# Optimization experiments

Measured on AMD Instinct MI355X. Metric: run time of the kernel, lower is better.

Reference implementation:

```python
import jax, jax.numpy as jnp
import numpy as np

D_MODEL = 256
N_HEADS = 8
D_FF = 1024
N_LAYERS = 6
INPUT_DIM = 2
EPS = 1e-5  # torch LayerNorm default


def _layer_norm(x, g, b):
    m = jnp.mean(x, axis=-1, keepdims=True)
    v = jnp.mean((x - m) ** 2, axis=-1, keepdims=True)
    return (x - m) / jnp.sqrt(v + EPS) * g + b


def setup_inputs() -> dict:
    key = jax.random.key(0)
    ks = jax.random.split(key, 8)
    f32 = jnp.float32

    def w(k, shape, fan_in):
        return jax.random.normal(k, shape, f32) * (1.0 / np.sqrt(fan_in))

    return {
        "x": jax.random.normal(ks[0], (8, 1024, INPUT_DIM), f32),
        "in_w": w(ks[1], (INPUT_DIM, D_MODEL), INPUT_DIM),
        "in_b": jnp.zeros((D_MODEL,), f32),
        "ln1_g": jnp.ones((D_MODEL,), f32),
        "ln1_b": jnp.zeros((D_MODEL,), f32),
        "qkv_w": w(ks[2], (D_MODEL, 3 * D_MODEL), D_MODEL),
        "qkv_b": jnp.zeros((3 * D_MODEL,), f32),
        "out_w": w(ks[3], (D_MODEL, D_MODEL), D_MODEL),
        "out_b": jnp.zeros((D_MODEL,), f32),
        "lna_g": jnp.ones((D_MODEL,), f32),
        "lna_b": jnp.zeros((D_MODEL,), f32),
        "ln2_g": jnp.ones((D_MODEL,), f32),
        "ln2_b": jnp.zeros((D_MODEL,), f32),
        "ff1_w": w(ks[4], (D_MODEL, D_FF), D_MODEL),
        "ff1_b": jnp.zeros((D_FF,), f32),
        "ff2_w": w(ks[5], (D_FF, D_MODEL), D_FF),
        "ff2_b": jnp.zeros((D_MODEL,), f32),
        "lnf_g": jnp.ones((D_MODEL,), f32),
        "lnf_b": jnp.zeros((D_MODEL,), f32),
    }


def reference(x, in_w, in_b, ln1_g, ln1_b, qkv_w, qkv_b, out_w, out_b,
              lna_g, lna_b, ln2_g, ln2_b, ff1_w, ff1_b, ff2_w, ff2_b,
              lnf_g, lnf_b):
    B, L, _ = x.shape
    dk = D_MODEL // N_HEADS
    scale = 1.0 / np.sqrt(dk)
    top_k = max(1, L // 4)

    # sinusoidal positional encoding [L, D]
    pos = jnp.arange(L, dtype=jnp.float32)[:, None]
    div = jnp.exp(jnp.arange(0, D_MODEL, 2, dtype=jnp.float32)
                  * (-np.log(10000.0) / D_MODEL))
    pe = jnp.zeros((L, D_MODEL), jnp.float32)
    pe = pe.at[:, 0::2].set(jnp.sin(pos * div))
    pe = pe.at[:, 1::2].set(jnp.cos(pos * div))

    h = x @ in_w + in_b + pe[None]  # [B, L, D]

    # VoformerEncoder reuses the SAME layer object -> shared weights, 6 passes
    for _ in range(N_LAYERS):
        # --- self-attention sublayer (pre-norm) ---
        s2 = _layer_norm(h, ln1_g, ln1_b)
        qkv = (s2 @ qkv_w + qkv_b).reshape(B, L, 3, N_HEADS, dk)
        q = qkv[:, :, 0].transpose(0, 2, 1, 3)  # [B, H, L, dk]
        k = qkv[:, :, 1].transpose(0, 2, 1, 3)
        v = qkv[:, :, 2].transpose(0, 2, 1, 3)

        scores = jnp.einsum('bhqd,bhkd->bhqk', q, k) * scale  # [B,H,L,L]
        # ProbSparse: keep only the per-row top-k scores
        thr = jax.lax.top_k(scores, top_k)[0][..., -1:]
        sparse = jnp.where(scores >= thr, scores, -jnp.inf)
        attn = jax.nn.softmax(sparse, axis=-1)
        o = jnp.einsum('bhqk,bhkd->bhqd', attn, v)
        o = o.transpose(0, 2, 1, 3).reshape(B, L, D_MODEL)
        o = o @ out_w + out_b
        # InformerAttention applies its own residual + LayerNorm
        attn_out = _layer_norm(o + s2, lna_g, lna_b)
        h = h + attn_out

        # --- FFN sublayer with Volatilite activation ---
        s2 = _layer_norm(h, ln2_g, ln2_b)
        f = s2 @ ff1_w + ff1_b  # [B, L, d_ff]
        mean_f = jnp.mean(f, axis=1, keepdims=True)
        vol = jnp.sqrt(jnp.mean((mean_f - f) ** 2, axis=1, keepdims=True))
        f = f * vol
        f = f @ ff2_w + ff2_b
        h = h + f

    return _layer_norm(h, lnf_g, lnf_b)
```

## Files before the change

kernel.cpp:

```cpp
#include <hip/hip_runtime.h>
#include <math.h>

#define D_MODEL 256
#define NH 8
#define DFF 1024
#define NLAYERS 6
#define B_ 8
#define L_ 1024
#define NR (B_*L_)
#define TOPK 256
#define LNEPS 1e-5f

typedef __attribute__((ext_vector_type(8))) short bf16x8;
typedef __attribute__((ext_vector_type(4))) float f32x4;

__device__ __forceinline__ float wsum(float v){
  #pragma unroll
  for(int o=32;o>0;o>>=1) v += __shfl_xor(v,o,64);
  return v;
}
__device__ __forceinline__ float wmax(float v){
  #pragma unroll
  for(int o=32;o>0;o>>=1) v = fmaxf(v,__shfl_xor(v,o,64));
  return v;
}
__device__ __forceinline__ short f2bf(float x){
  unsigned u = __float_as_uint(x);
  u += 0x7fffu + ((u>>16)&1u);
  return (short)(u>>16);
}
__device__ __forceinline__ float bf2f(short s){
  return __uint_as_float(((unsigned)(unsigned short)s)<<16);
}
__device__ __forceinline__ void g2l(const short* g, short* l){
  __builtin_amdgcn_global_load_lds(
      (const __attribute__((address_space(1))) unsigned int*)g,
      (__attribute__((address_space(3))) unsigned int*)l,
      16, 0, 0);
}

__global__ __launch_bounds__(256) void embed_kernel(
    const float* __restrict__ x, const float* __restrict__ in_w,
    const float* __restrict__ in_b, float* __restrict__ h)
{
  int tid = blockIdx.x*256 + threadIdx.x;
  int n  = tid >> 6;
  int d0 = (tid & 63) << 2;
  int l  = n & (L_-1);
  float x0 = x[2*n], x1 = x[2*n+1];
  const float kf = -0.07195578415606394f;
  float pe[4];
  #pragma unroll
  for(int ii=0; ii<2; ++ii){
    int i = (d0>>1) + ii;
    float dv  = expf((float)i * kf);
    float ang = (float)l * dv;
    pe[2*ii]   = sinf(ang);
    pe[2*ii+1] = cosf(ang);
  }
  float4 w0 = *(const float4*)(in_w + d0);
  float4 w1 = *(const float4*)(in_w + D_MODEL + d0);
  float4 bb = *(const float4*)(in_b + d0);
  float4 o;
  o.x = x0*w0.x + x1*w1.x + bb.x + pe[0];
  o.y = x0*w0.y + x1*w1.y + bb.y + pe[1];
  o.z = x0*w0.z + x1*w1.z + bb.z + pe[2];
  o.w = x0*w0.w + x1*w1.w + bb.w + pe[3];
  *(float4*)(h + (size_t)n*D_MODEL + d0) = o;
}

__global__ __launch_bounds__(256) void wcvt(
    const float* __restrict__ W, short* __restrict__ WT, int N, int kshift)
{
  int idx = blockIdx.x*256 + threadIdx.x;
  int K = 1<<kshift;
  if (idx >= N*K) return;
  int n = idx >> kshift, k = idx & (K-1);
  WT[idx] = f2bf(W[(size_t)k*N + n]);
}

template<int OM>
__global__ __launch_bounds__(256) void ln_kernel(
    const float* __restrict__ in, const float* __restrict__ g,
    const float* __restrict__ b, float* __restrict__ out,
    short* __restrict__ outb)
{
  int wave = threadIdx.x >> 6, lane = threadIdx.x & 63;
  int row = blockIdx.x*4 + wave;
  float4 v = ((const float4*)(in + (size_t)row*D_MODEL))[lane];
  float s  = v.x+v.y+v.z+v.w;
  float sq = v.x*v.x+v.y*v.y+v.z*v.z+v.w*v.w;
  s = wsum(s); sq = wsum(sq);
  float mean = s*(1.f/D_MODEL);
  float var  = sq*(1.f/D_MODEL) - mean*mean;
  float rstd = 1.f/sqrtf(var + LNEPS);
  float4 gv = ((const float4*)g)[lane];
  float4 bv = ((const float4*)b)[lane];
  float4 o;
  o.x = (v.x-mean)*rstd*gv.x + bv.x;
  o.y = (v.y-mean)*rstd*gv.y + bv.y;
  o.z = (v.z-mean)*rstd*gv.z + bv.z;
  o.w = (v.w-mean)*rstd*gv.w + bv.w;
  if (OM == 0 || OM == 1){
    ((float4*)(out + (size_t)row*D_MODEL))[lane] = o;
  }
  if (OM == 3){
    float4* op = (float4*)(out + (size_t)row*D_MODEL) + lane;
    float4 hv = *op;
    o.x+=hv.x; o.y+=hv.y; o.z+=hv.z; o.w+=hv.w;
    *op = o;
  }
  if (OM == 1 || OM == 2){
    short4 s4; s4.x=f2bf(o.x); s4.y=f2bf(o.y); s4.z=f2bf(o.z); s4.w=f2bf(o.w);
    *(short4*)(outb + (size_t)row*D_MODEL + lane*4) = s4;
  }
}

template<int MODE>
__global__ __launch_bounds__(256) void mfma_gemm(
    const short* __restrict__ A, const short* __restrict__ BT,
    const float* __restrict__ bias, const float* __restrict__ resid,
    float* __restrict__ Cf, short* __restrict__ Cb, short* __restrict__ Vt,
    int N, int K)
{
  __shared__ __align__(16) short As[128*32];
  __shared__ __align__(16) short Bs[64*32];
  const int t = threadIdx.x, wv = t>>6, lane = t&63;
  const int r16 = lane&15, quad = lane>>4;
  const int m0 = blockIdx.y*128, n0 = blockIdx.x*64;
  const int ia0 = wv*128 + lane, ia1 = ia0 + 64;
  const int ib  = wv*64 + lane;
  const short* Ab = A  + (size_t)m0*K;
  const short* Bb = BT + (size_t)n0*K;
  const f32x4 z = {0.f,0.f,0.f,0.f};
  f32x4 acc[2][4];
  #pragma unroll
  for (int i=0;i<2;++i)
    #pragma unroll
    for (int j=0;j<4;++j) acc[i][j] = z;

  for (int k0 = 0; k0 < K; k0 += 32){
    __syncthreads();
    g2l(Ab + (size_t)(ia0>>2)*K + k0 + (ia0&3)*8, As + ia0*8);
    g2l(Ab + (size_t)(ia1>>2)*K + k0 + (ia1&3)*8, As + ia1*8);
    g2l(Bb + (size_t)(ib>>2)*K  + k0 + (ib&3)*8,  Bs + ib*8);
    __syncthreads();
    bf16x8 af0 = *(const bf16x8*)(As + ((wv*32      + r16)*32 + quad*8));
    bf16x8 af1 = *(const bf16x8*)(As + ((wv*32 + 16 + r16)*32 + quad*8));
    bf16x8 bf[4];
    #pragma unroll
    for (int ct=0; ct<4; ++ct)
      bf[ct] = *(const bf16x8*)(Bs + ((ct*16 + r16)*32 + quad*8));
    #pragma unroll
    for (int ct=0; ct<4; ++ct){
      acc[0][ct] = __builtin_amdgcn_mfma_f32_16x16x32_bf16(af0, bf[ct], acc[0][ct], 0,0,0);
      acc[1][ct] = __builtin_amdgcn_mfma_f32_16x16x32_bf16(af1, bf[ct], acc[1][ct], 0,0,0);
    }
  }

  #pragma unroll
  for (int rt=0; rt<2; ++rt){
    const int mb = m0 + wv*32 + rt*16 + quad*4;
    #pragma unroll
    for (int ct=0; ct<4; ++ct){
      const int n = n0 + ct*16 + r16;
      const float bv = bias[n];
      if (MODE == 0){
        if (n < 512){
          int region = n>>8, hh = (n>>5)&7, d = n&31;
          #pragma unroll
          for (int r=0;r<4;++r){
            int l = mb + r;
            size_t base = (((size_t)(region*64 + (l>>10)*8 + hh))*1024 + (l&1023))*32 + d;
            Cb[base] = f2bf(acc[rt][ct][r] + bv);
          }
        } else {
          int dv = n - 512, hh = dv>>5, d = dv&31;
          int b = mb>>10, lloc = mb&1023;
          size_t base = (((size_t)(b*8 + hh))*32 + d)*1024 + lloc;
          short4 s4;
          s4.x = f2bf(acc[rt][ct][0] + bv); s4.y = f2bf(acc[rt][ct][1] + bv);
          s4.z = f2bf(acc[rt][ct][2] + bv); s4.w = f2bf(acc[rt][ct][3] + bv);
          *(short4*)(Vt + base) = s4;
        }
      } else {
        #pragma unroll
        for (int r=0;r<4;++r){
          size_t off = (size_t)(mb + r)*N + n;
          float c = acc[rt][ct][r] + bv;
          if (MODE == 1) Cf[off] = c + resid[off];
          if (MODE == 2) Cb[off] = f2bf(c);
          if (MODE == 3) Cf[off] += c;
        }
      }
    }
  }
}

__global__ __launch_bounds__(256,4) void attn_mfma(
    const short* __restrict__ qkbf, const short* __restrict__ vT,
    short* __restrict__ ob)
{
  __shared__ __align__(16) short sc16[16*1024];
  const int t = threadIdx.x, wv = t>>6, lane = t&63;
  const int r16 = lane&15, quad = lane>>4;
  const int bh = blockIdx.x >> 6, qt = blockIdx.x & 63;

  bf16x8 aq = *(const bf16x8*)(qkbf + ((size_t)bh*1024 + qt*16 + r16)*32 + quad*8);
  const short* kb = qkbf + (size_t)(64 + bh)*1024*32;

  bf16x8 bk[16];
  #pragma unroll
  for (int tt=0; tt<16; ++tt)
    bk[tt] = *(const bf16x8*)(kb + (size_t)(wv*256 + tt*16 + r16)*32 + quad*8);
  #pragma unroll
  for (int tt=0; tt<16; ++tt){
    f32x4 c = {0.f,0.f,0.f,0.f};
    c = __builtin_amdgcn_mfma_f32_16x16x32_bf16(aq, bk[tt], c, 0, 0, 0);
    int key = wv*256 + tt*16 + r16;
    #pragma unroll
    for (int r=0;r<4;++r){
      int row = quad*4 + r;
      sc16[row*1024 + (key ^ ((row&7)<<3))] = f2bf(c[r]);
    }
  }
  __syncthreads();

  const float SC2 = 0.25500529485087056f;
  for (int rr=0; rr<4; ++rr){
    int row = wv*4 + rr;
    int s = (row&7)<<3;
    float scv[16]; int key[16];
    #pragma unroll
    for (int i=0;i<16;++i){
      short hsh = sc16[row*1024 + ((i*64+lane) ^ s)];
      scv[i] = bf2f(hsh);
      int u = (int)(unsigned short)hsh;
      key[i] = (u & 0x8000) ? (u ^ 0xFFFF) : (u | 0x8000);
    }
    int lo=0, hi=65536;
    while (hi - lo > 1){
      int mid = (lo+hi)>>1;
      int cnt = 0;
      #pragma unroll
      for (int i=0;i<16;++i)
        cnt += (int)__popcll(__ballot(key[i] >= mid));
      if (cnt >= TOPK) lo = mid; else hi = mid;
    }
    const int thr = lo;
    float mx = scv[0];
    #pragma unroll
    for (int i=1;i<16;++i) mx = fmaxf(mx, scv[i]);
    mx = wmax(mx);
    float sum = 0.f, w[16];
    #pragma unroll
    for (int i=0;i<16;++i){
      float e = (key[i] >= thr) ? exp2f((scv[i]-mx)*SC2) : 0.f;
      w[i] = e; sum += e;
    }
    sum = wsum(sum);
    const float inv = 1.f/sum;
    #pragma unroll
    for (int i=0;i<16;++i)
      sc16[row*1024 + ((i*64+lane) ^ s)] = f2bf(w[i]*inv);
  }
  __syncthreads();

  const short* vb = vT + (size_t)bh*32*1024;
  bf16x8 bvv[16];
  #pragma unroll
  for (int tt=0; tt<8; ++tt){
    int k0 = wv*256 + tt*32;
    #pragma unroll
    for (int n=0;n<2;++n)
      bvv[tt*2+n] = *(const bf16x8*)(vb + (size_t)(n*16 + r16)*1024 + k0 + quad*8);
  }
  f32x4 oa0 = {0.f,0.f,0.f,0.f}, oa1 = {0.f,0.f,0.f,0.f};
  #pragma unroll
  for (int tt=0; tt<8; ++tt){
    int k0 = wv*256 + tt*32;
    bf16x8 af = *(const bf16x8*)(sc16 + r16*1024 + ((k0 + quad*8) ^ ((r16&7)<<3)));
    oa0 = __builtin_amdgcn_mfma_f32_16x16x32_bf16(af, bvv[tt*2+0], oa0, 0, 0, 0);
    oa1 = __builtin_amdgcn_mfma_f32_16x16x32_bf16(af, bvv[tt*2+1], oa1, 0, 0, 0);
  }
  __syncthreads();
  float* po = (float*)sc16;
  #pragma unroll
  for (int r=0;r<4;++r){
    po[wv*512 + (quad*4+r)*32 +      r16] = oa0[r];
    po[wv*512 + (quad*4+r)*32 + 16 + r16] = oa1[r];
  }
  __syncthreads();
  int e = t*2;
  float v0 = po[e]   + po[512+e]   + po[1024+e]   + po[1536+e];
  float v1 = po[e+1] + po[512+e+1] + po[1024+e+1] + po[1536+e+1];
  int q = e>>5, d = e&31;
  int b = bh>>3, hh = bh&7;
  size_t off = ((size_t)(b*1024 + qt*16 + q))*256 + hh*32 + d;
  short2 s2o; s2o.x = f2bf(v0); s2o.y = f2bf(v1);
  *(short2*)(ob + off) = s2o;
}

__global__ __launch_bounds__(512) void vol_scale(short* __restrict__ f)
{
  __shared__ float ps[8][64], pq[8][64], vs[64];
  int b = blockIdx.x >> 4, cb = blockIdx.x & 15;
  int cl = threadIdx.x & 63, sl = threadIdx.x >> 6;
  int col = cb*64 + cl;
  short* fb = f + (size_t)b*L_*DFF + col;
  float s = 0.f, sq = 0.f;
  for (int l = sl*128; l < sl*128+128; ++l){
    float v = bf2f(fb[(size_t)l*DFF]);
    s += v; sq += v*v;
  }
  ps[sl][cl] = s; pq[sl][cl] = sq;
  __syncthreads();
  if (threadIdx.x < 64){
    float st=0.f, qt=0.f;
    #pragma unroll
    for (int i=0;i<8;++i){ st += ps[i][cl]; qt += pq[i][cl]; }
    float mean = st*(1.f/L_);
    float var  = qt*(1.f/L_) - mean*mean;
    vs[cl] = sqrtf(fmaxf(var, 0.f));
  }
  __syncthreads();
  float vv = vs[cl];
  for (int l = sl*128; l < sl*128+128; ++l){
    size_t o = (size_t)l*DFF;
    fb[o] = f2bf(bf2f(fb[o]) * vv);
  }
}

extern "C" void kernel_launch(void* const* d_in, const int* in_sizes, int n_in,
                              void* d_out, int out_size, void* d_ws, size_t ws_size,
                              hipStream_t stream) {
  const float* x     = (const float*)d_in[0];
  const float* in_w  = (const float*)d_in[1];
  const float* in_b  = (const float*)d_in[2];
  const float* ln1_g = (const float*)d_in[3];
  const float* ln1_b = (const float*)d_in[4];
  const float* qkv_w = (const float*)d_in[5];
  const float* qkv_b = (const float*)d_in[6];
  const float* out_w = (const float*)d_in[7];
  const float* out_b = (const float*)d_in[8];
  const float* lna_g = (const float*)d_in[9];
  const float* lna_b = (const float*)d_in[10];
  const float* ln2_g = (const float*)d_in[11];
  const float* ln2_b = (const float*)d_in[12];
  const float* ff1_w = (const float*)d_in[13];
  const float* ff1_b = (const float*)d_in[14];
  const float* ff2_w = (const float*)d_in[15];
  const float* ff2_b = (const float*)d_in[16];
  const float* lnf_g = (const float*)d_in[17];
  const float* lnf_b = (const float*)d_in[18];
  float* out = (float*)d_out;

  char* ws = (char*)d_ws;
  float* h     = (float*)(ws);
  float* s2    = (float*)(ws + (size_t)( 8<<20));
  short* s2b   = (short*)(ws + (size_t)(16<<20));
  short* qkbf  = (short*)(ws + (size_t)(20<<20));
  short* vTb   = (short*)(ws + (size_t)(28<<20));
  short* ob_b  = (short*)(ws + (size_t)(32<<20));
  short* f     = (short*)(ws + (size_t)(20<<20));
  float* tb    = (float*)(ws + (size_t)(36<<20));
  short* qkvwT = (short*)(ws + (size_t)(45<<20));
  short* outwT = (short*)(ws + (size_t)(45<<20) + 393216);
  short* ff1wT = (short*)(ws + (size_t)(45<<20) + 393216 + 131072);
  short* ff2wT = (short*)(ws + (size_t)(45<<20) + 393216 + 131072 + 524288);

  embed_kernel<<<NR*64/256, 256, 0, stream>>>(x, in_w, in_b, h);
  wcvt<<< 768, 256, 0, stream>>>(qkv_w, qkvwT,  768, 8);
  wcvt<<< 256, 256, 0, stream>>>(out_w, outwT,  256, 8);
  wcvt<<<1024, 256, 0, stream>>>(ff1_w, ff1wT, 1024, 8);
  wcvt<<<1024, 256, 0, stream>>>(ff2_w, ff2wT,  256, 10);

  for (int layer = 0; layer < NLAYERS; ++layer){
    ln_kernel<1><<<NR/4, 256, 0, stream>>>(h, ln1_g, ln1_b, s2, s2b);
    {
      dim3 g(768/64, NR/128);
      mfma_gemm<0><<<g, 256, 0, stream>>>(s2b, qkvwT, qkv_b, nullptr,
                                          nullptr, qkbf, vTb, 768, 256);
    }
    attn_mfma<<<64*64, 256, 0, stream>>>(qkbf, vTb, ob_b);
    {
      dim3 g(256/64, NR/128);
      mfma_gemm<1><<<g, 256, 0, stream>>>(ob_b, outwT, out_b, s2,
                                          tb, nullptr, nullptr, 256, 256);
    }
    ln_kernel<3><<<NR/4, 256, 0, stream>>>(tb, lna_g, lna_b, h, nullptr);
    ln_kernel<2><<<NR/4, 256, 0, stream>>>(h, ln2_g, ln2_b, nullptr, s2b);
    {
      dim3 g(1024/64, NR/128);
      mfma_gemm<2><<<g, 256, 0, stream>>>(s2b, ff1wT, ff1_b, nullptr,
                                          nullptr, f, nullptr, 1024, 256);
    }
    vol_scale<<<B_*16, 512, 0, stream>>>(f);
    {
      dim3 g(256/64, NR/128);
      mfma_gemm<3><<<g, 256, 0, stream>>>(f, ff2wT, ff2_b, nullptr,
                                          h, nullptr, nullptr, 256, 1024);
    }
  }
  ln_kernel<0><<<NR/4, 256, 0, stream>>>(h, lnf_g, lnf_b, out, nullptr);
}
```

Measured before the change: 1.362 ms.

## Fuse out-projection with residual and both LayerNorms, restructure top-k softmax attention

A new gemm_ln kernel does the attention output projection, adds the residual, applies the attention LayerNorm, adds the result into h and computes the next LN2 in its epilogue. This replaces one GEMM plus two LayerNorm launches and drops the fp32 s2 buffer; the residual is now read from the bf16 normalized input. The attention kernel now has each wave process four rows at once. It uses a 16-step bitwise threshold search on integer sort keys with interleaved ballots, defers softmax normalization to the PV output, stores scores in a transposed swizzled layout and remaps block indices. Risks: precision loss from the bf16 residual, and gemm_ln launches only 128 blocks with a non-pipelined K loop.

```diff
diff --git a/kernel.cpp b/kernel.cpp
--- a/kernel.cpp
+++ b/kernel.cpp
@@ -1,4 +1,5 @@
 #include <hip/hip_runtime.h>
+#include <hip/hip_bf16.h>
 #include <math.h>
 
 #define D_MODEL 256
@@ -19,11 +20,6 @@
   for(int o=32;o>0;o>>=1) v += __shfl_xor(v,o,64);
   return v;
 }
-__device__ __forceinline__ float wmax(float v){
-  #pragma unroll
-  for(int o=32;o>0;o>>=1) v = fmaxf(v,__shfl_xor(v,o,64));
-  return v;
-}
 __device__ __forceinline__ short f2bf(float x){
   unsigned u = __float_as_uint(x);
   u += 0x7fffu + ((u>>16)&1u);
@@ -31,6 +27,18 @@
 }
 __device__ __forceinline__ float bf2f(short s){
   return __uint_as_float(((unsigned)(unsigned short)s)<<16);
+}
+__device__ __forceinline__ unsigned pk2bf(float a, float b){
+  __hip_bfloat162 h = __float22bfloat162_rn(make_float2(a,b));
+  unsigned u; __builtin_memcpy(&u, &h, 4);
+  return u;
+}
+__device__ __forceinline__ int sortkey(unsigned u){
+  return (u & 0x8000u) ? (int)(u ^ 0xFFFFu) : (int)(u | 0x8000u);
+}
+__device__ __forceinline__ float kinvf(int k){
+  unsigned u = (k & 0x8000) ? ((unsigned)k ^ 0x8000u) : ((unsigned)k ^ 0xFFFFu);
+  return __uint_as_float(u << 16);
 }
 __device__ __forceinline__ void g2l(const short* g, short* l){
   __builtin_amdgcn_global_load_lds(
@@ -101,25 +109,19 @@
   o.y = (v.y-mean)*rstd*gv.y + bv.y;
   o.z = (v.z-mean)*rstd*gv.z + bv.z;
   o.w = (v.w-mean)*rstd*gv.w + bv.w;
-  if (OM == 0 || OM == 1){
+  if (OM == 0){
     ((float4*)(out + (size_t)row*D_MODEL))[lane] = o;
   }
-  if (OM == 3){
-    float4* op = (float4*)(out + (size_t)row*D_MODEL) + lane;
-    float4 hv = *op;
-    o.x+=hv.x; o.y+=hv.y; o.z+=hv.z; o.w+=hv.w;
-    *op = o;
-  }
-  if (OM == 1 || OM == 2){
-    short4 s4; s4.x=f2bf(o.x); s4.y=f2bf(o.y); s4.z=f2bf(o.z); s4.w=f2bf(o.w);
-    *(short4*)(outb + (size_t)row*D_MODEL + lane*4) = s4;
+  if (OM == 2){
+    uint2 pk; pk.x = pk2bf(o.x, o.y); pk.y = pk2bf(o.z, o.w);
+    *(uint2*)(outb + (size_t)row*D_MODEL + lane*4) = pk;
   }
 }
 
 template<int MODE>
 __global__ __launch_bounds__(256) void mfma_gemm(
     const short* __restrict__ A, const short* __restrict__ BT,
-    const float* __restrict__ bias, const float* __restrict__ resid,
+    const float* __restrict__ bias,
     float* __restrict__ Cf, short* __restrict__ Cb, short* __restrict__ Vt,
     int N, int K)
 {
@@ -178,17 +180,16 @@
           int dv = n - 512, hh = dv>>5, d = dv&31;
           int b = mb>>10, lloc = mb&1023;
           size_t base = (((size_t)(b*8 + hh))*32 + d)*1024 + lloc;
-          short4 s4;
-          s4.x = f2bf(acc[rt][ct][0] + bv); s4.y = f2bf(acc[rt][ct][1] + bv);
-          s4.z = f2bf(acc[rt][ct][2] + bv); s4.w = f2bf(acc[rt][ct][3] + bv);
-          *(short4*)(Vt + base) = s4;
+          uint2 pk;
+          pk.x = pk2bf(acc[rt][ct][0] + bv, acc[rt][ct][1] + bv);
+          pk.y = pk2bf(acc[rt][ct][2] + bv, acc[rt][ct][3] + bv);
+          *(uint2*)(Vt + base) = pk;
         }
       } else {
         #pragma unroll
         for (int r=0;r<4;++r){
           size_t off = (size_t)(mb + r)*N + n;
           float c = acc[rt][ct][r] + bv;
-          if (MODE == 1) Cf[off] = c + resid[off];
           if (MODE == 2) Cb[off] = f2bf(c);
           if (MODE == 3) Cf[off] += c;
         }
@@ -197,6 +198,85 @@
   }
 }
 
+template<int RES>
+__global__ __launch_bounds__(256) void gemm_ln(
+    const short* __restrict__ A, const short* __restrict__ BT,
+    const float* __restrict__ bias, const short* __restrict__ residb,
+    const float* __restrict__ ga, const float* __restrict__ ba,
+    const float* __restrict__ g2, const float* __restrict__ b2,
+    float* __restrict__ h, short* __restrict__ s2b, int K)
+{
+  __shared__ __align__(16) short As[64*32];
+  __shared__ __align__(16) short Bs[256*32];
+  const int t = threadIdx.x, wv = t>>6, lane = t&63;
+  const int r16 = lane&15, quad = lane>>4;
+  const int m0 = blockIdx.x*64;
+  const short* Ab = A + (size_t)m0*K;
+  const f32x4 z = {0.f,0.f,0.f,0.f};
+  f32x4 acc[16];
+  #pragma unroll
+  for (int i=0;i<16;++i) acc[i] = z;
+
+  for (int k0 = 0; k0 < K; k0 += 32){
+    __syncthreads();
+    g2l(Ab + (size_t)(t>>2)*K + k0 + (t&3)*8, As + t*8);
+    #pragma unroll
+    for (int j=0;j<4;++j){
+      int c = j*256 + t;
+      g2l(BT + (size_t)(c>>2)*K + k0 + (c&3)*8, Bs + c*8);
+    }
+    __syncthreads();
+    bf16x8 af = *(const bf16x8*)(As + ((wv*16 + r16)*32 + quad*8));
+    #pragma unroll
+    for (int ct=0; ct<16; ++ct){
+      bf16x8 bfr = *(const bf16x8*)(Bs + ((ct*16 + r16)*32 + quad*8));
+      acc[ct] = __builtin_amdgcn_mfma_f32_16x16x32_bf16(af, bfr, acc[ct], 0,0,0);
+    }
+  }
+
+  #pragma unroll
+  for (int r=0;r<4;++r){
+    const int R = m0 + wv*16 + quad*4 + r;
+    float tv[16];
+    #pragma unroll
+    for (int ct=0;ct<16;++ct)
+      tv[ct] = acc[ct][r] + bias[ct*16 + r16];
+    if (RES){
+      #pragma unroll
+      for (int ct=0;ct<16;++ct)
+        tv[ct] += bf2f(residb[(size_t)R*256 + ct*16 + r16]);
+      float s=0.f, sq=0.f;
+      #pragma unroll
+      for (int ct=0;ct<16;++ct){ s += tv[ct]; sq += tv[ct]*tv[ct]; }
+      #pragma unroll
+      for (int m=1;m<16;m<<=1){ s += __shfl_xor(s,m,64); sq += __shfl_xor(sq,m,64); }
+      float mean = s*(1.f/256.f);
+      float var  = sq*(1.f/256.f) - mean*mean;
+      float rstd = 1.f/sqrtf(var + LNEPS);
+      #pragma unroll
+      for (int ct=0;ct<16;++ct)
+        tv[ct] = (tv[ct]-mean)*rstd*ga[ct*16+r16] + ba[ct*16+r16];
+    }
+    float hv[16];
+    float s2=0.f, sq2=0.f;
+    #pragma unroll
+    for (int ct=0;ct<16;++ct){
+      size_t off = (size_t)R*256 + ct*16 + r16;
+      hv[ct] = h[off] + tv[ct];
+      h[off] = hv[ct];
+      s2 += hv[ct]; sq2 += hv[ct]*hv[ct];
+    }
+    #pragma unroll
+    for (int m=1;m<16;m<<=1){ s2 += __shfl_xor(s2,m,64); sq2 += __shfl_xor(sq2,m,64); }
+    float m2 = s2*(1.f/256.f);
+    float v2 = sq2*(1.f/256.f) - m2*m2;
+    float r2 = 1.f/sqrtf(v2 + LNEPS);
+    #pragma unroll
+    for (int ct=0;ct<16;++ct)
+      s2b[(size_t)R*256 + ct*16 + r16] = f2bf((hv[ct]-m2)*r2*g2[ct*16+r16] + b2[ct*16+r16]);
+  }
+}
+
 __global__ __launch_bounds__(256,4) void attn_mfma(
     const short* __restrict__ qkbf, const short* __restrict__ vT,
     short* __restrict__ ob)
@@ -204,7 +284,9 @@
   __shared__ __align__(16) short sc16[16*1024];
   const int t = threadIdx.x, wv = t>>6, lane = t&63;
   const int r16 = lane&15, quad = lane>>4;
-  const int bh = blockIdx.x >> 6, qt = blockIdx.x & 63;
+  const int blk = blockIdx.x;
+  const int bh = (blk & 7)*8 + ((blk>>3)&7);
+  const int qt = blk >> 6;
 
   bf16x8 aq = *(const bf16x8*)(qkbf + ((size_t)bh*1024 + qt*16 + r16)*32 + quad*8);
   const short* kb = qkbf + (size_t)(64 + bh)*1024*32;
@@ -217,53 +299,94 @@
   for (int tt=0; tt<16; ++tt){
     f32x4 c = {0.f,0.f,0.f,0.f};
     c = __builtin_amdgcn_mfma_f32_16x16x32_bf16(aq, bk[tt], c, 0, 0, 0);
-    int key = wv*256 + tt*16 + r16;
-    #pragma unroll
-    for (int r=0;r<4;++r){
-      int row = quad*4 + r;
-      sc16[row*1024 + (key ^ ((row&7)<<3))] = f2bf(c[r]);
-    }
-  }
-  __syncthreads();
-
+    const int key = wv*256 + tt*16 + r16;
+    const int g = ((key>>2) ^ (key>>4)) & 3;
+    uint2 pk;
+    pk.x = pk2bf(c[0], c[1]);
+    pk.y = pk2bf(c[2], c[3]);
+    *(uint2*)(sc16 + key*16 + ((quad ^ g)<<2)) = pk;
+  }
+  __syncthreads();
+
+  uint2 rw[16];
+  #pragma unroll
+  for (int i=0;i<16;++i){
+    int k = i*64 + lane;
+    int g = ((k>>2) ^ (k>>4)) & 3;
+    rw[i] = *(const uint2*)(sc16 + k*16 + ((wv ^ g)<<2));
+  }
+  __syncthreads();
+
+  int k0a[16], k1a[16], k2a[16], k3a[16];
+  #pragma unroll
+  for (int i=0;i<16;++i){
+    k0a[i] = sortkey(rw[i].x & 0xFFFFu);
+    k1a[i] = sortkey(rw[i].x >> 16);
+    k2a[i] = sortkey(rw[i].y & 0xFFFFu);
+    k3a[i] = sortkey(rw[i].y >> 16);
+  }
+  int mx0=k0a[0], mx1=k1a[0], mx2=k2a[0], mx3=k3a[0];
+  #pragma unroll
+  for (int i=1;i<16;++i){
+    mx0 = (k0a[i]>mx0)?k0a[i]:mx0;
+    mx1 = (k1a[i]>mx1)?k1a[i]:mx1;
+    mx2 = (k2a[i]>mx2)?k2a[i]:mx2;
+    mx3 = (k3a[i]>mx3)?k3a[i]:mx3;
+  }
+  #pragma unroll
+  for (int o=32;o>0;o>>=1){
+    int a;
+    a = __shfl_xor(mx0,o,64); mx0 = (a>mx0)?a:mx0;
+    a = __shfl_xor(mx1,o,64); mx1 = (a>mx1)?a:mx1;
+    a = __shfl_xor(mx2,o,64); mx2 = (a>mx2)?a:mx2;
+    a = __shfl_xor(mx3,o,64); mx3 = (a>mx3)?a:mx3;
+  }
+  int lo0=0, lo1=0, lo2=0, lo3=0;
+  #pragma unroll
+  for (int bit=15; bit>=0; --bit){
+    const int m0 = lo0 + (1<<bit), m1 = lo1 + (1<<bit);
+    const int m2 = lo2 + (1<<bit), m3 = lo3 + (1<<bit);
+    int c0=0, c1=0, c2=0, c3=0;
+    #pragma unroll
+    for (int i=0;i<16;++i){
+      c0 += (int)__popcll(__ballot(k0a[i] >= m0));
+      c1 += (int)__popcll(__ballot(k1a[i] >= m1));
+      c2 += (int)__popcll(__ballot(k2a[i] >= m2));
+      c3 += (int)__popcll(__ballot(k3a[i] >= m3));
+    }
+    if (c0 >= TOPK) lo0 = m0;
+    if (c1 >= TOPK) lo1 = m1;
+    if (c2 >= TOPK) lo2 = m2;
+    if (c3 >= TOPK) lo3 = m3;
+  }
   const float SC2 = 0.25500529485087056f;
-  for (int rr=0; rr<4; ++rr){
-    int row = wv*4 + rr;
-    int s = (row&7)<<3;
-    float scv[16]; int key[16];
-    #pragma unroll
-    for (int i=0;i<16;++i){
-      short hsh = sc16[row*1024 + ((i*64+lane) ^ s)];
-      scv[i] = bf2f(hsh);
-      int u = (int)(unsigned short)hsh;
-      key[i] = (u & 0x8000) ? (u ^ 0xFFFF) : (u | 0x8000);
-    }
-    int lo=0, hi=65536;
-    while (hi - lo > 1){
-      int mid = (lo+hi)>>1;
-      int cnt = 0;
-      #pragma unroll
-      for (int i=0;i<16;++i)
-        cnt += (int)__popcll(__ballot(key[i] >= mid));
-      if (cnt >= TOPK) lo = mid; else hi = mid;
-    }
-    const int thr = lo;
-    float mx = scv[0];
-    #pragma unroll
-    for (int i=1;i<16;++i) mx = fmaxf(mx, scv[i]);
-    mx = wmax(mx);
-    float sum = 0.f, w[16];
-    #pragma unroll
-    for (int i=0;i<16;++i){
-      float e = (key[i] >= thr) ? exp2f((scv[i]-mx)*SC2) : 0.f;
-      w[i] = e; sum += e;
-    }
-    sum = wsum(sum);
-    const float inv = 1.f/sum;
-    #pragma unroll
-    for (int i=0;i<16;++i)
-      sc16[row*1024 + ((i*64+lane) ^ s)] = f2bf(w[i]*inv);
-  }
+  const float nm0 = -kinvf(mx0)*SC2, nm1 = -kinvf(mx1)*SC2;
+  const float nm2 = -kinvf(mx2)*SC2, nm3 = -kinvf(mx3)*SC2;
+  const int r0 = wv*4;
+  short* w0 = sc16 + (r0  )*1024;
+  short* w1 = sc16 + (r0+1)*1024;
+  short* w2 = sc16 + (r0+2)*1024;
+  short* w3 = sc16 + (r0+3)*1024;
+  const int s0 = ((r0  )&7)<<3, s1 = ((r0+1)&7)<<3;
+  const int s2 = ((r0+2)&7)<<3, s3 = ((r0+3)&7)<<3;
+  float sum0=0.f, sum1=0.f, sum2=0.f, sum3=0.f;
+  #pragma unroll
+  for (int i=0;i<16;++i){
+    const int k = i*64 + lane;
+    float e0 = (k0a[i] >= lo0) ? exp2f(fmaf(kinvf(k0a[i]), SC2, nm0)) : 0.f;
+    float e1 = (k1a[i] >= lo1) ? exp2f(fmaf(kinvf(k1a[i]), SC2, nm1)) : 0.f;
+    float e2 = (k2a[i] >= lo2) ? exp2f(fmaf(kinvf(k2a[i]), SC2, nm2)) : 0.f;
+    float e3 = (k3a[i] >= lo3) ? exp2f(fmaf(kinvf(k3a[i]), SC2, nm3)) : 0.f;
+    sum0 += e0; sum1 += e1; sum2 += e2; sum3 += e3;
+    w0[k ^ s0] = f2bf(e0);
+    w1[k ^ s1] = f2bf(e1);
+    w2[k ^ s2] = f2bf(e2);
+    w3[k ^ s3] = f2bf(e3);
+  }
+  sum0 = wsum(sum0); sum1 = wsum(sum1);
+  sum2 = wsum(sum2); sum3 = wsum(sum3);
+  const float sq_ = (quad==0)?sum0 : (quad==1)?sum1 : (quad==2)?sum2 : sum3;
+  const float invq = 1.f/sq_;
   __syncthreads();
 
   const short* vb = vT + (size_t)bh*32*1024;
@@ -275,11 +398,12 @@
     for (int n=0;n<2;++n)
       bvv[tt*2+n] = *(const bf16x8*)(vb + (size_t)(n*16 + r16)*1024 + k0 + quad*8);
   }
+  const int sA = (r16&7) << 3;
   f32x4 oa0 = {0.f,0.f,0.f,0.f}, oa1 = {0.f,0.f,0.f,0.f};
   #pragma unroll
   for (int tt=0; tt<8; ++tt){
     int k0 = wv*256 + tt*32;
-    bf16x8 af = *(const bf16x8*)(sc16 + r16*1024 + ((k0 + quad*8) ^ ((r16&7)<<3)));
+    bf16x8 af = *(const bf16x8*)(sc16 + r16*1024 + ((k0 + quad*8) ^ sA));
     oa0 = __builtin_amdgcn_mfma_f32_16x16x32_bf16(af, bvv[tt*2+0], oa0, 0, 0, 0);
     oa1 = __builtin_amdgcn_mfma_f32_16x16x32_bf16(af, bvv[tt*2+1], oa1, 0, 0, 0);
   }
@@ -297,8 +421,7 @@
   int q = e>>5, d = e&31;
   int b = bh>>3, hh = bh&7;
   size_t off = ((size_t)(b*1024 + qt*16 + q))*256 + hh*32 + d;
-  short2 s2o; s2o.x = f2bf(v0); s2o.y = f2bf(v1);
-  *(short2*)(ob + off) = s2o;
+  *(unsigned*)(ob + off) = pk2bf(v0*invq, v1*invq);
 }
 
 __global__ __launch_bounds__(512) void vol_scale(short* __restrict__ f)
@@ -357,17 +480,15 @@
 
   char* ws = (char*)d_ws;
   float* h     = (float*)(ws);
-  float* s2    = (float*)(ws + (size_t)( 8<<20));
-  short* s2b   = (short*)(ws + (size_t)(16<<20));
-  short* qkbf  = (short*)(ws + (size_t)(20<<20));
-  short* vTb   = (short*)(ws + (size_t)(28<<20));
-  short* ob_b  = (short*)(ws + (size_t)(32<<20));
-  short* f     = (short*)(ws + (size_t)(20<<20));
-  float* tb    = (float*)(ws + (size_t)(36<<20));
-  short* qkvwT = (short*)(ws + (size_t)(45<<20));
-  short* outwT = (short*)(ws + (size_t)(45<<20) + 393216);
-  short* ff1wT = (short*)(ws + (size_t)(45<<20) + 393216 + 131072);
-  short* ff2wT = (short*)(ws + (size_t)(45<<20) + 393216 + 131072 + 524288);
+  short* s2b   = (short*)(ws + (size_t)( 8<<20));
+  short* qkbf  = (short*)(ws + (size_t)(12<<20));
+  short* vTb   = (short*)(ws + (size_t)(20<<20));
+  short* ob_b  = (short*)(ws + (size_t)(24<<20));
+  short* f     = (short*)(ws + (size_t)(12<<20));
+  short* qkvwT = (short*)(ws + (size_t)(28<<20));
+  short* outwT = (short*)(ws + (size_t)(28<<20) + 393216);
+  short* ff1wT = (short*)(ws + (size_t)(28<<20) + 393216 + 131072);
+  short* ff2wT = (short*)(ws + (size_t)(28<<20) + 393216 + 131072 + 524288);
 
   embed_kernel<<<NR*64/256, 256, 0, stream>>>(x, in_w, in_b, h);
   wcvt<<< 768, 256, 0, stream>>>(qkv_w, qkvwT,  768, 8);
@@ -375,32 +496,31 @@
   wcvt<<<1024, 256, 0, stream>>>(ff1_w, ff1wT, 1024, 8);
   wcvt<<<1024, 256, 0, stream>>>(ff2_w, ff2wT,  256, 10);
 
+  ln_kernel<2><<<NR/4, 256, 0, stream>>>(h, ln1_g, ln1_b, nullptr, s2b);
+
   for (int layer = 0; layer < NLAYERS; ++layer){
-    ln_kernel<1><<<NR/4, 256, 0, stream>>>(h, ln1_g, ln1_b, s2, s2b);
     {
       dim3 g(768/64, NR/128);
-      mfma_gemm<0><<<g, 256, 0, stream>>>(s2b, qkvwT, qkv_b, nullptr,
+      mfma_gemm<0><<<g, 256, 0, stream>>>(s2b, qkvwT, qkv_b,
                                           nullptr, qkbf, vTb, 768, 256);
     }
     attn_mfma<<<64*64, 256, 0, stream>>>(qkbf, vTb, ob_b);
-    {
-      dim3 g(256/64, NR/128);
-      mfma_gemm<1><<<g, 256, 0, stream>>>(ob_b, outwT, out_b, s2,
-                                          tb, nullptr, nullptr, 256, 256);
-    }
-    ln_kernel<3><<<NR/4, 256, 0, stream>>>(tb, lna_g, lna_b, h, nullptr);
-    ln_kernel<2><<<NR/4, 256, 0, stream>>>(h, ln2_g, ln2_b, nullptr, s2b);
+    gemm_ln<1><<<NR/64, 256, 0, stream>>>(ob_b, outwT, out_b, s2b,
+                                          lna_g, lna_b, ln2_g, ln2_b,
+                                          h, s2b, 256);
     {
       dim3 g(1024/64, NR/128);
-      mfma_gemm<2><<<g, 256, 0, stream>>>(s2b, ff1wT, ff1_b, nullptr,
+      mfma_gemm<2><<<g, 256, 0, stream>>>(s2b, ff1wT, ff1_b,
                                           nullptr, f, nullptr, 1024, 256);
     }
     vol_scale<<<B_*16, 512, 0, stream>>>(f);
     {
       dim3 g(256/64, NR/128);
-      mfma_gemm<3><<<g, 256, 0, stream>>>(f, ff2wT, ff2_b, nullptr,
+      mfma_gemm<3><<<g, 256, 0, stream>>>(f, ff2wT, ff2_b,
                                           h, nullptr, nullptr, 256, 1024);
     }
+    if (layer < NLAYERS-1)
+      ln_kernel<2><<<NR/4, 256, 0, stream>>>(h, ln1_g, ln1_b, nullptr, s2b);
   }
   ln_kernel<0><<<NR/4, 256, 0, stream>>>(h, lnf_g, lnf_b, out, nullptr);
 }
```

Measured after the change: 1.569 ms. 15.3% more time.
